# Optimization experiments

Hardware: AMD Instinct MI355X
Metric: run time of the kernel (lower is better)

## Reference

```python
import jax, jax.numpy as jnp
import numpy as np

T, B, D, H = 256, 128, 512, 512


def setup_inputs() -> dict:
    key = jax.random.key(0)
    ks = jax.random.split(key, 9)
    s = 0.01  # init scale from the original module
    return {
        "X": jax.random.normal(ks[0], (T, B, D), dtype=jnp.float32),
        "Wa_x": s * jax.random.normal(ks[1], (D, H), dtype=jnp.float32),
        "Wi_x": s * jax.random.normal(ks[2], (D, H), dtype=jnp.float32),
        "Wf_x": s * jax.random.normal(ks[3], (D, H), dtype=jnp.float32),
        "Wo_x": s * jax.random.normal(ks[4], (D, H), dtype=jnp.float32),
        "Wa_h": s * jax.random.normal(ks[5], (H, H), dtype=jnp.float32),
        "Wi_h": s * jax.random.normal(ks[6], (H, H), dtype=jnp.float32),
        "Wf_h": s * jax.random.normal(ks[7], (H, H), dtype=jnp.float32),
        "Wo_h": s * jax.random.normal(ks[8], (H, H), dtype=jnp.float32),
        "ba": jnp.zeros((H,), dtype=jnp.float32),
        "bi": jnp.zeros((H,), dtype=jnp.float32),
        "bf": jnp.zeros((H,), dtype=jnp.float32),
        "bo": jnp.zeros((H,), dtype=jnp.float32),
    }


def reference(X, Wa_x, Wi_x, Wf_x, Wo_x, Wa_h, Wi_h, Wf_h, Wo_h, ba, bi, bf, bo):
    # Concatenate gate weights/biases so each step does one fused matmul per
    # source (input / hidden). Math is identical to four separate matmuls.
    Wx = jnp.concatenate([Wa_x, Wi_x, Wf_x, Wo_x], axis=1)  # [D, 4H]
    Wh = jnp.concatenate([Wa_h, Wi_h, Wf_h, Wo_h], axis=1)  # [H, 4H]
    b = jnp.concatenate([ba, bi, bf, bo], axis=0)            # [4H]
    n = ba.shape[0]

    # Precompute input projections for all timesteps in one big matmul: [T,B,4H]
    Xg = jnp.einsum('tbd,dg->tbg', X, Wx) + b

    def step(carry, xg):
        h_prev, s_prev = carry
        g = xg + h_prev @ Wh  # note: t=0 uses h_prev=0, matching the original
        a = jnp.tanh(g[:, 0 * n:1 * n])
        i = jax.nn.sigmoid(g[:, 1 * n:2 * n])
        f = jax.nn.sigmoid(g[:, 2 * n:3 * n])
        o = jax.nn.sigmoid(g[:, 3 * n:4 * n])
        s = a * i + s_prev * f  # t=0: s_prev=0 -> s = a*i, matching original
        h = jnp.tanh(s) * o
        return (h, s), h

    h0 = jnp.zeros((X.shape[1], n), dtype=X.dtype)
    s0 = jnp.zeros((X.shape[1], n), dtype=X.dtype)
    _, outputs = jax.lax.scan(step, (h0, s0), Xg)  # [T, B, H]
    return outputs
```

## Files before the change

### kernel.cpp

```cpp
#include <hip/hip_runtime.h>


#define TT 256
#define BB 128
#define DD 512
#define HH 512
#define KK 1024
#define NBLK 256

typedef __bf16 bf16x8 __attribute__((ext_vector_type(8)));
typedef float f32x4 __attribute__((ext_vector_type(4)));
typedef unsigned short u16x8 __attribute__((ext_vector_type(8)));
typedef unsigned long long u64;

union h128 { u64 q[2]; bf16x8 v; };

__device__ __forceinline__ unsigned short f2bf(float f) {
  unsigned b = __builtin_bit_cast(unsigned, f);
  return (unsigned short)((b + 0x7fffu + ((b >> 16) & 1u)) >> 16);
}
__device__ __forceinline__ float fexp(float x) {
  return __builtin_amdgcn_exp2f(x * 1.4426950408889634f);
}
__device__ __forceinline__ float fsig(float x) {
  return __builtin_amdgcn_rcpf(1.0f + fexp(-x));
}
__device__ __forceinline__ float ftanh(float x) {
  return 2.0f * fsig(2.0f * x) - 1.0f;
}

__global__ __launch_bounds__(256) void convert_x_kernel(const float* __restrict__ X,
                                                        unsigned short* __restrict__ Xbf) {
  size_t i = (size_t)blockIdx.x * 256 + threadIdx.x;
  const float4* src = (const float4*)X + i * 2;
  float4 v0 = src[0], v1 = src[1];
  u16x8 o;
  o[0] = f2bf(v0.x); o[1] = f2bf(v0.y); o[2] = f2bf(v0.z); o[3] = f2bf(v0.w);
  o[4] = f2bf(v1.x); o[5] = f2bf(v1.y); o[6] = f2bf(v1.z); o[7] = f2bf(v1.w);
  ((u16x8*)Xbf)[i] = o;
}

__global__ __launch_bounds__(256) void build_wt_kernel(
    const float* __restrict__ Wax, const float* __restrict__ Wix,
    const float* __restrict__ Wfx, const float* __restrict__ Wox,
    const float* __restrict__ Wah, const float* __restrict__ Wih,
    const float* __restrict__ Wfh, const float* __restrict__ Woh,
    unsigned short* __restrict__ WT) {
  __shared__ float tile[64][65];
  int bid = blockIdx.x;
  int q  = bid >> 7;
  int jt = (bid >> 4) & 7;
  int kt = bid & 15;
  const float* Wx[4] = {Wax, Wix, Wfx, Wox};
  const float* Wh[4] = {Wah, Wih, Wfh, Woh};
  const float* src = (kt < 8) ? Wx[q] : Wh[q];
  int k0 = (kt & 7) * 64;
  int j0 = jt * 64;
  int tid = threadIdx.x;
#pragma unroll
  for (int e = 0; e < 16; ++e) {
    int lin = e * 256 + tid;
    int kk = lin >> 6, jj = lin & 63;
    tile[kk][jj] = src[(size_t)(k0 + kk) * HH + j0 + jj];
  }
  __syncthreads();
#pragma unroll
  for (int e = 0; e < 16; ++e) {
    int lin = e * 256 + tid;
    int jj = lin >> 6, kk = lin & 63;
    WT[(size_t)(q * HH + j0 + jj) * KK + kt * 64 + kk] = f2bf(tile[kk][jj]);
  }
}

__global__ __launch_bounds__(256, 1) void lstm_main(
    const unsigned short* __restrict__ Xbf,
    const unsigned short* __restrict__ WT,
    const float* __restrict__ ba, const float* __restrict__ bi,
    const float* __restrict__ bfg, const float* __restrict__ bo,
    unsigned short* __restrict__ hbuf,
    float* __restrict__ out,
    int* __restrict__ cnt) {
  const int tid  = threadIdx.x;
  const int bid  = blockIdx.x;
  const int lane = tid & 63;
  const int wave = tid >> 6;
  const int rb = bid >> 5;
  const int cb = bid & 31;
  const int l15 = lane & 15;
  const int lk8 = (lane >> 4) * 8;
  const int rbase = rb * 16;
  const int colg = cb * 16 + l15;
  const int wk = wave * 128;

  bf16x8 wf[4][8];
#pragma unroll
  for (int g = 0; g < 4; ++g) {
    const unsigned short* wg = WT + (size_t)(g * HH + colg) * KK + lk8;
#pragma unroll
    for (int c = 0; c < 8; ++c) {
      int kb = (c < 4) ? (wk + c * 32) : (DD + wk + (c - 4) * 32);
      wf[g][c] = *(const bf16x8*)(wg + kb);
    }
  }

  const int el_row = tid >> 4;
  const int el_col = tid & 15;
  const int el_colg = cb * 16 + el_col;
  const int el_rowg = rbase + el_row;
  const float b0 = ba[el_colg], b1 = bi[el_colg], b2 = bfg[el_colg], b3 = bo[el_colg];
  const int lsrc = (el_row >> 2) * 16 + el_col;
  const int rsrc = el_row & 3;

  const unsigned short* xbase = Xbf + (size_t)(rbase + l15) * DD + wk + lk8;
  const size_t hrow = (size_t)(rbase + l15) * HH + wk + lk8;
  const size_t hstore_el = (size_t)el_rowg * HH + el_colg;

  __shared__ f32x4 part[2][4][4][64];

  float s_c = 0.f;

  for (int t = 0; t < TT; ++t) {
    const unsigned short* xt = xbase + (size_t)t * BB * DD;
    bf16x8 ax0 = *(const bf16x8*)(xt);
    bf16x8 ax1 = *(const bf16x8*)(xt + 32);
    bf16x8 ax2 = *(const bf16x8*)(xt + 64);
    bf16x8 ax3 = *(const bf16x8*)(xt + 96);

    f32x4 acc[4];
#pragma unroll
    for (int g = 0; g < 4; ++g) {
      f32x4 z = {0.f, 0.f, 0.f, 0.f};
      acc[g] = __builtin_amdgcn_mfma_f32_16x16x32_bf16(ax0, wf[g][0], z, 0, 0, 0);
      acc[g] = __builtin_amdgcn_mfma_f32_16x16x32_bf16(ax1, wf[g][1], acc[g], 0, 0, 0);
      acc[g] = __builtin_amdgcn_mfma_f32_16x16x32_bf16(ax2, wf[g][2], acc[g], 0, 0, 0);
      acc[g] = __builtin_amdgcn_mfma_f32_16x16x32_bf16(ax3, wf[g][3], acc[g], 0, 0, 0);
    }

    if (t > 0) {
      if (tid == 0) {
        while (__hip_atomic_load(&cnt[rb * TT + (t - 1)], __ATOMIC_RELAXED,
                                 __HIP_MEMORY_SCOPE_AGENT) < 32) {}
      }
      __syncthreads();
    }

    const u64* hp = (const u64*)(hbuf + (size_t)((t & 1) ^ 1) * BB * HH + hrow);
    h128 u0, u1, u2, u3;
    u0.q[0] = __hip_atomic_load(hp +  0, __ATOMIC_RELAXED, __HIP_MEMORY_SCOPE_AGENT);
    u0.q[1] = __hip_atomic_load(hp +  1, __ATOMIC_RELAXED, __HIP_MEMORY_SCOPE_AGENT);
    u1.q[0] = __hip_atomic_load(hp +  8, __ATOMIC_RELAXED, __HIP_MEMORY_SCOPE_AGENT);
    u1.q[1] = __hip_atomic_load(hp +  9, __ATOMIC_RELAXED, __HIP_MEMORY_SCOPE_AGENT);
    u2.q[0] = __hip_atomic_load(hp + 16, __ATOMIC_RELAXED, __HIP_MEMORY_SCOPE_AGENT);
    u2.q[1] = __hip_atomic_load(hp + 17, __ATOMIC_RELAXED, __HIP_MEMORY_SCOPE_AGENT);
    u3.q[0] = __hip_atomic_load(hp + 24, __ATOMIC_RELAXED, __HIP_MEMORY_SCOPE_AGENT);
    u3.q[1] = __hip_atomic_load(hp + 25, __ATOMIC_RELAXED, __HIP_MEMORY_SCOPE_AGENT);

#pragma unroll
    for (int g = 0; g < 4; ++g) {
      acc[g] = __builtin_amdgcn_mfma_f32_16x16x32_bf16(u0.v, wf[g][4], acc[g], 0, 0, 0);
      acc[g] = __builtin_amdgcn_mfma_f32_16x16x32_bf16(u1.v, wf[g][5], acc[g], 0, 0, 0);
      acc[g] = __builtin_amdgcn_mfma_f32_16x16x32_bf16(u2.v, wf[g][6], acc[g], 0, 0, 0);
      acc[g] = __builtin_amdgcn_mfma_f32_16x16x32_bf16(u3.v, wf[g][7], acc[g], 0, 0, 0);
    }

    const int pb = t & 1;
#pragma unroll
    for (int g = 0; g < 4; ++g) part[pb][wave][g][lane] = acc[g];
    __syncthreads();

    float g0 = b0, g1 = b1, g2 = b2, g3 = b3;
#pragma unroll
    for (int w = 0; w < 4; ++w) {
      g0 += ((const float*)&part[pb][w][0][lsrc])[rsrc];
      g1 += ((const float*)&part[pb][w][1][lsrc])[rsrc];
      g2 += ((const float*)&part[pb][w][2][lsrc])[rsrc];
      g3 += ((const float*)&part[pb][w][3][lsrc])[rsrc];
    }
    float av = ftanh(g0);
    float iv = fsig(g1);
    float fv = fsig(g2);
    float ov = fsig(g3);
    s_c = av * iv + s_c * fv;
    float hv = ftanh(s_c) * ov;

    out[(size_t)t * BB * HH + hstore_el] = hv;

    unsigned mybf = (unsigned)f2bf(hv);
    unsigned nxbf = (unsigned)__shfl_down((int)mybf, 1);
    if ((tid & 1) == 0) {
      unsigned pack = mybf | (nxbf << 16);
      unsigned* dst = (unsigned*)(hbuf + (size_t)pb * BB * HH + hstore_el);
      __hip_atomic_store(dst, pack, __ATOMIC_RELAXED, __HIP_MEMORY_SCOPE_AGENT);
    }

    if (t == TT - 1) break;

    __syncthreads();
    if (tid == 0) {
      __hip_atomic_fetch_add(&cnt[rb * TT + t], 1, __ATOMIC_RELAXED,
                             __HIP_MEMORY_SCOPE_AGENT);
    }
  }
}

extern "C" void kernel_launch(void* const* d_in, const int* in_sizes, int n_in,
                              void* d_out, int out_size, void* d_ws, size_t ws_size,
                              hipStream_t stream) {
  const float* X   = (const float*)d_in[0];
  const float* Wax = (const float*)d_in[1];
  const float* Wix = (const float*)d_in[2];
  const float* Wfx = (const float*)d_in[3];
  const float* Wox = (const float*)d_in[4];
  const float* Wah = (const float*)d_in[5];
  const float* Wih = (const float*)d_in[6];
  const float* Wfh = (const float*)d_in[7];
  const float* Woh = (const float*)d_in[8];
  const float* ba  = (const float*)d_in[9];
  const float* bi  = (const float*)d_in[10];
  const float* bf  = (const float*)d_in[11];
  const float* bo  = (const float*)d_in[12];
  float* out = (float*)d_out;

  char* ws = (char*)d_ws;
  unsigned short* Xbf  = (unsigned short*)ws;
  unsigned short* WT   = (unsigned short*)(ws + 33554432);
  unsigned short* hbuf = (unsigned short*)(ws + 33554432 + 4194304);
  int* cnt             = (int*)(ws + 33554432 + 4194304 + 262144);

  hipMemsetAsync(hbuf, 0, 262144 + 8192, stream);

  convert_x_kernel<<<8192, 256, 0, stream>>>(X, Xbf);
  build_wt_kernel<<<512, 256, 0, stream>>>(Wax, Wix, Wfx, Wox, Wah, Wih, Wfh, Woh, WT);
  lstm_main<<<NBLK, 256, 0, stream>>>(Xbf, WT, ba, bi, bf, bo, hbuf, out, cnt);
}
```

Baseline: 780.7 us.

## Replace per-step counter barrier with tagged h values polled directly

The per-row-block atomic counter barrier, with its __syncthreads and fetch_add, is replaced by a scheme where each h element is stored as a 32-bit word pairing a timestep tag with its bf16 value. Consumers poll their own h operands until every tag matches the current step, then unpack the values for the MFMAs. This removes the counter round trip and the block-wide syncs that wrapped it. In exchange, each h read is twice as wide, the workspace doubles, and every thread spins on global loads.

```diff
diff --git a/kernel.cpp b/kernel.cpp
--- a/kernel.cpp
+++ b/kernel.cpp
@@ -11,9 +11,6 @@
 typedef __bf16 bf16x8 __attribute__((ext_vector_type(8)));
 typedef float f32x4 __attribute__((ext_vector_type(4)));
 typedef unsigned short u16x8 __attribute__((ext_vector_type(8)));
-typedef unsigned long long u64;
-
-union h128 { u64 q[2]; bf16x8 v; };
 
 __device__ __forceinline__ unsigned short f2bf(float f) {
   unsigned b = __builtin_bit_cast(unsigned, f);
@@ -77,9 +74,8 @@
     const unsigned short* __restrict__ WT,
     const float* __restrict__ ba, const float* __restrict__ bi,
     const float* __restrict__ bfg, const float* __restrict__ bo,
-    unsigned short* __restrict__ hbuf,
-    float* __restrict__ out,
-    int* __restrict__ cnt) {
+    unsigned* __restrict__ hpair,
+    float* __restrict__ out) {
   const int tid  = threadIdx.x;
   const int bid  = blockIdx.x;
   const int lane = tid & 63;
@@ -112,7 +108,7 @@
   const int rsrc = el_row & 3;
 
   const unsigned short* xbase = Xbf + (size_t)(rbase + l15) * DD + wk + lk8;
-  const size_t hrow = (size_t)(rbase + l15) * HH + wk + lk8;
+  const size_t hrowp = (size_t)(rbase + l15) * HH + wk + lk8;
   const size_t hstore_el = (size_t)el_rowg * HH + el_colg;
 
   __shared__ f32x4 part[2][4][4][64];
@@ -137,30 +133,42 @@
     }
 
     if (t > 0) {
-      if (tid == 0) {
-        while (__hip_atomic_load(&cnt[rb * TT + (t - 1)], __ATOMIC_RELAXED,
-                                 __HIP_MEMORY_SCOPE_AGENT) < 32) {}
+      const unsigned tagw = (unsigned)t;
+      const unsigned* hp = hpair + (size_t)((t & 1) ^ 1) * BB * HH + hrowp;
+      unsigned q[4][8];
+      while (true) {
+#pragma unroll
+        for (int c = 0; c < 4; ++c)
+#pragma unroll
+          for (int j = 0; j < 8; ++j)
+            q[c][j] = __hip_atomic_load(hp + c * 32 + j, __ATOMIC_RELAXED,
+                                        __HIP_MEMORY_SCOPE_AGENT);
+        unsigned bad = 0;
+#pragma unroll
+        for (int c = 0; c < 4; ++c)
+#pragma unroll
+          for (int j = 0; j < 8; ++j)
+            bad |= (q[c][j] ^ tagw);
+        if (__all((bad & 0xffffu) == 0u)) break;
+        __builtin_amdgcn_s_sleep(1);
       }
-      __syncthreads();
-    }
-
-    const u64* hp = (const u64*)(hbuf + (size_t)((t & 1) ^ 1) * BB * HH + hrow);
-    h128 u0, u1, u2, u3;
-    u0.q[0] = __hip_atomic_load(hp +  0, __ATOMIC_RELAXED, __HIP_MEMORY_SCOPE_AGENT);
-    u0.q[1] = __hip_atomic_load(hp +  1, __ATOMIC_RELAXED, __HIP_MEMORY_SCOPE_AGENT);
-    u1.q[0] = __hip_atomic_load(hp +  8, __ATOMIC_RELAXED, __HIP_MEMORY_SCOPE_AGENT);
-    u1.q[1] = __hip_atomic_load(hp +  9, __ATOMIC_RELAXED, __HIP_MEMORY_SCOPE_AGENT);
-    u2.q[0] = __hip_atomic_load(hp + 16, __ATOMIC_RELAXED, __HIP_MEMORY_SCOPE_AGENT);
-    u2.q[1] = __hip_atomic_load(hp + 17, __ATOMIC_RELAXED, __HIP_MEMORY_SCOPE_AGENT);
-    u3.q[0] = __hip_atomic_load(hp + 24, __ATOMIC_RELAXED, __HIP_MEMORY_SCOPE_AGENT);
-    u3.q[1] = __hip_atomic_load(hp + 25, __ATOMIC_RELAXED, __HIP_MEMORY_SCOPE_AGENT);
-
-#pragma unroll
-    for (int g = 0; g < 4; ++g) {
-      acc[g] = __builtin_amdgcn_mfma_f32_16x16x32_bf16(u0.v, wf[g][4], acc[g], 0, 0, 0);
-      acc[g] = __builtin_amdgcn_mfma_f32_16x16x32_bf16(u1.v, wf[g][5], acc[g], 0, 0, 0);
-      acc[g] = __builtin_amdgcn_mfma_f32_16x16x32_bf16(u2.v, wf[g][6], acc[g], 0, 0, 0);
-      acc[g] = __builtin_amdgcn_mfma_f32_16x16x32_bf16(u3.v, wf[g][7], acc[g], 0, 0, 0);
+      bf16x8 hf[4];
+#pragma unroll
+      for (int c = 0; c < 4; ++c) {
+        unsigned w0 = (q[c][0] >> 16) | (q[c][1] & 0xffff0000u);
+        unsigned w1 = (q[c][2] >> 16) | (q[c][3] & 0xffff0000u);
+        unsigned w2 = (q[c][4] >> 16) | (q[c][5] & 0xffff0000u);
+        unsigned w3 = (q[c][6] >> 16) | (q[c][7] & 0xffff0000u);
+        uint4 u = make_uint4(w0, w1, w2, w3);
+        hf[c] = __builtin_bit_cast(bf16x8, u);
+      }
+#pragma unroll
+      for (int g = 0; g < 4; ++g) {
+        acc[g] = __builtin_amdgcn_mfma_f32_16x16x32_bf16(hf[0], wf[g][4], acc[g], 0, 0, 0);
+        acc[g] = __builtin_amdgcn_mfma_f32_16x16x32_bf16(hf[1], wf[g][5], acc[g], 0, 0, 0);
+        acc[g] = __builtin_amdgcn_mfma_f32_16x16x32_bf16(hf[2], wf[g][6], acc[g], 0, 0, 0);
+        acc[g] = __builtin_amdgcn_mfma_f32_16x16x32_bf16(hf[3], wf[g][7], acc[g], 0, 0, 0);
+      }
     }
 
     const int pb = t & 1;
@@ -183,23 +191,13 @@
     s_c = av * iv + s_c * fv;
     float hv = ftanh(s_c) * ov;
 
+    if (t < TT - 1) {
+      unsigned pairv = (unsigned)(t + 1) | ((unsigned)f2bf(hv) << 16);
+      __hip_atomic_store(&hpair[(size_t)pb * BB * HH + hstore_el], pairv,
+                         __ATOMIC_RELAXED, __HIP_MEMORY_SCOPE_AGENT);
+    }
+
     out[(size_t)t * BB * HH + hstore_el] = hv;
-
-    unsigned mybf = (unsigned)f2bf(hv);
-    unsigned nxbf = (unsigned)__shfl_down((int)mybf, 1);
-    if ((tid & 1) == 0) {
-      unsigned pack = mybf | (nxbf << 16);
-      unsigned* dst = (unsigned*)(hbuf + (size_t)pb * BB * HH + hstore_el);
-      __hip_atomic_store(dst, pack, __ATOMIC_RELAXED, __HIP_MEMORY_SCOPE_AGENT);
-    }
-
-    if (t == TT - 1) break;
-
-    __syncthreads();
-    if (tid == 0) {
-      __hip_atomic_fetch_add(&cnt[rb * TT + t], 1, __ATOMIC_RELAXED,
-                             __HIP_MEMORY_SCOPE_AGENT);
-    }
   }
 }
 
@@ -222,14 +220,13 @@
   float* out = (float*)d_out;
 
   char* ws = (char*)d_ws;
-  unsigned short* Xbf  = (unsigned short*)ws;
-  unsigned short* WT   = (unsigned short*)(ws + 33554432);
-  unsigned short* hbuf = (unsigned short*)(ws + 33554432 + 4194304);
-  int* cnt             = (int*)(ws + 33554432 + 4194304 + 262144);
-
-  hipMemsetAsync(hbuf, 0, 262144 + 8192, stream);
+  unsigned short* Xbf = (unsigned short*)ws;
+  unsigned short* WT  = (unsigned short*)(ws + 33554432);
+  unsigned* hpair     = (unsigned*)(ws + 33554432 + 4194304);
+
+  hipMemsetAsync(hpair, 0, 524288, stream);
 
   convert_x_kernel<<<8192, 256, 0, stream>>>(X, Xbf);
   build_wt_kernel<<<512, 256, 0, stream>>>(Wax, Wix, Wfx, Wox, Wah, Wih, Wfh, Woh, WT);
-  lstm_main<<<NBLK, 256, 0, stream>>>(Xbf, WT, ba, bi, bf, bo, hbuf, out, cnt);
-}
+  lstm_main<<<NBLK, 256, 0, stream>>>(Xbf, WT, ba, bi, bf, bo, hpair, out);
+}
```

After: 1.390 ms. +78.1%, slower.
